# Optimization experiments

Hardware: AMD Instinct MI355X
Metric: run time of the kernel (lower is better)

## Reference

```python
import jax, jax.numpy as jnp
import numpy as np

B, T, C, DK = 4096, 33, 512, 64  # batch, seq (== encoder_block_size), n_embd, d_k


def setup_inputs() -> dict:
    key = jax.random.key(0)
    k1, k2, k3, k4 = jax.random.split(key, 4)
    w_scale = 1.0 / np.sqrt(C).astype(np.float32)
    x = jax.random.normal(k1, (B, T, C), dtype=jnp.float32)
    Wq = jax.random.normal(k2, (DK, C), dtype=jnp.float32) * w_scale
    Wk = jax.random.normal(k3, (DK, C), dtype=jnp.float32) * w_scale
    Wv = jax.random.normal(k4, (DK, C), dtype=jnp.float32) * w_scale
    return {"x": x, "Wq": Wq, "Wk": Wk, "Wv": Wv}


def reference(x, Wq, Wk, Wv):
    # nn.Linear(n_embd, d_k, bias=False): y = x @ W.T
    q = jnp.einsum('btc,dc->btd', x, Wq)  # [B,T,DK]
    k = jnp.einsum('btc,dc->btd', x, Wk)
    v = jnp.einsum('btc,dc->btd', x, Wv)
    # NOTE: original scales by C**-0.5 (n_embd), not d_k**-0.5 — keep faithful.
    wei = jnp.einsum('btd,bsd->bts', q, k) * (C ** -0.5)  # [B,T,T]
    tril = jnp.tril(jnp.ones((T, T), dtype=bool))
    wei = jnp.where(tril, wei, -jnp.inf)
    wei = jax.nn.softmax(wei, axis=-1)
    # dropout p=0.0 -> identity
    out = jnp.einsum('bts,bsd->btd', wei, v)  # [B,T,DK]
    return out
```

## Files before the change

### kernel.cpp

```cpp
#include <hip/hip_runtime.h>
#include <hip/hip_bf16.h>


typedef __attribute__((ext_vector_type(8))) short bf16x8;
typedef __attribute__((ext_vector_type(4))) float floatx4;

#define NB 4096
#define TT 33
#define CC 512

#define CHS 136
#define QS  72
#define OFF_C0 0
#define OFF_C1 8976
#define OFF_Q  0
#define OFF_K  4752
#define OFF_VT 9504
#define OFF_P  18720
#define SMEM_BYTES 25632

__device__ __forceinline__ ushort f2b(float f) {
    union { __hip_bfloat16 h; ushort u; } cv;
    cv.h = __float2bfloat16(f);
    return cv.u;
}
__device__ __forceinline__ int imin(int a, int b) { return a < b ? a : b; }

__device__ __forceinline__ bf16x8 load8_b(const ushort* p) { return *(const bf16x8*)p; }
__device__ __forceinline__ bf16x8 load8_f(const float* p) {
    float4 f0 = *(const float4*)p;
    float4 f1 = *(const float4*)(p + 4);
    bf16x8 r;
    r[0] = (short)f2b(f0.x); r[1] = (short)f2b(f0.y);
    r[2] = (short)f2b(f0.z); r[3] = (short)f2b(f0.w);
    r[4] = (short)f2b(f1.x); r[5] = (short)f2b(f1.y);
    r[6] = (short)f2b(f1.z); r[7] = (short)f2b(f1.w);
    return r;
}

__global__ void conv_w_kernel(const float* __restrict__ Wq,
                              const float* __restrict__ Wk,
                              const float* __restrict__ Wv,
                              ushort* __restrict__ wb) {
    const float* src = (blockIdx.y == 0) ? Wq : (blockIdx.y == 1) ? Wk : Wv;
    int i = (blockIdx.x * 256 + threadIdx.x) * 4;
    float4 f = *(const float4*)&src[i];
    ushort4 u;
    u.x = f2b(f.x); u.y = f2b(f.y); u.z = f2b(f.z); u.w = f2b(f.w);
    *(ushort4*)&wb[(size_t)blockIdx.y * 32768 + i] = u;
}

template <bool USE_WS>
__global__ __launch_bounds__(256, 4) void head_kernel(
    const float* __restrict__ x,
    const ushort* __restrict__ wb,
    const float* __restrict__ Wqf,
    const float* __restrict__ Wkf,
    const float* __restrict__ Wvf,
    float* __restrict__ out)
{
    __shared__ __align__(16) char smem[SMEM_BYTES];
    ushort* xc0  = (ushort*)(smem + OFF_C0);
    ushort* xc1  = (ushort*)(smem + OFF_C1);
    ushort* q_s  = (ushort*)(smem + OFF_Q);
    ushort* k_s  = (ushort*)(smem + OFF_K);
    ushort* vT_s = (ushort*)(smem + OFF_VT);

    const int b    = blockIdx.x;
    const int tid  = threadIdx.x;
    const int lane = tid & 63;
    const int wave = tid >> 6;
    const int l15  = lane & 15;
    const int quad = lane >> 4;

    const float* xg = x + (size_t)b * (TT * CC);

    int nidx[3];
    const ushort* wrow_b[3];
    const float*  wrow_f[3];
    #pragma unroll
    for (int nl = 0; nl < 3; nl++) {
        int n = wave * 3 + nl;
        nidx[nl] = n;
        int mat = n >> 2;
        int row = (n & 3) * 16 + l15;
        if (USE_WS) {
            wrow_b[nl] = wb + (size_t)mat * 32768 + (size_t)row * CC;
            wrow_f[nl] = nullptr;
        } else {
            const float* Wf = (mat == 0) ? Wqf : (mat == 1) ? Wkf : Wvf;
            wrow_f[nl] = Wf + (size_t)row * CC;
            wrow_b[nl] = nullptr;
        }
    }

    float4 buf[5];
    auto LOADCHUNK = [&](int c) {
        #pragma unroll
        for (int j = 0; j < 5; j++) {
            int i = tid + j * 256;
            if (i < 1056) {
                int r = i >> 5, c4 = i & 31;
                buf[j] = ((const float4*)xg)[r * 128 + c * 32 + c4];
            }
        }
    };
    auto WRITECHUNK = [&](ushort* dst) {
        #pragma unroll
        for (int j = 0; j < 5; j++) {
            int i = tid + j * 256;
            if (i < 1056) {
                int r = i >> 5, c4 = i & 31;
                ushort4 u;
                u.x = f2b(buf[j].x); u.y = f2b(buf[j].y);
                u.z = f2b(buf[j].z); u.w = f2b(buf[j].w);
                *(ushort4*)&dst[r * CHS + c4 * 4] = u;
            }
        }
    };

    LOADCHUNK(0);
    WRITECHUNK(xc0);
    __syncthreads();

    floatx4 acc[3][3] = {};
    const int r0 = l15, r1 = 16 + l15, r2 = 32;

    #pragma unroll
    for (int c = 0; c < 4; c++) {
        if (c < 3) LOADCHUNK(c + 1);
        const ushort* xs = (c & 1) ? xc1 : xc0;
        #pragma unroll
        for (int ksl = 0; ksl < 4; ksl++) {
            int col  = ksl * 32 + quad * 8;
            int wcol = c * 128 + col;
            bf16x8 a0 = *(const bf16x8*)&xs[r0 * CHS + col];
            bf16x8 a1 = *(const bf16x8*)&xs[r1 * CHS + col];
            bf16x8 a2 = *(const bf16x8*)&xs[r2 * CHS + col];
            bf16x8 b0 = USE_WS ? load8_b(&wrow_b[0][wcol]) : load8_f(&wrow_f[0][wcol]);
            bf16x8 b1 = USE_WS ? load8_b(&wrow_b[1][wcol]) : load8_f(&wrow_f[1][wcol]);
            bf16x8 b2 = USE_WS ? load8_b(&wrow_b[2][wcol]) : load8_f(&wrow_f[2][wcol]);
            acc[0][0] = __builtin_amdgcn_mfma_f32_16x16x32_bf16(a0, b0, acc[0][0], 0, 0, 0);
            acc[1][0] = __builtin_amdgcn_mfma_f32_16x16x32_bf16(a1, b0, acc[1][0], 0, 0, 0);
            acc[2][0] = __builtin_amdgcn_mfma_f32_16x16x32_bf16(a2, b0, acc[2][0], 0, 0, 0);
            acc[0][1] = __builtin_amdgcn_mfma_f32_16x16x32_bf16(a0, b1, acc[0][1], 0, 0, 0);
            acc[1][1] = __builtin_amdgcn_mfma_f32_16x16x32_bf16(a1, b1, acc[1][1], 0, 0, 0);
            acc[2][1] = __builtin_amdgcn_mfma_f32_16x16x32_bf16(a2, b1, acc[2][1], 0, 0, 0);
            acc[0][2] = __builtin_amdgcn_mfma_f32_16x16x32_bf16(a0, b2, acc[0][2], 0, 0, 0);
            acc[1][2] = __builtin_amdgcn_mfma_f32_16x16x32_bf16(a1, b2, acc[1][2], 0, 0, 0);
            acc[2][2] = __builtin_amdgcn_mfma_f32_16x16x32_bf16(a2, b2, acc[2][2], 0, 0, 0);
        }
        if (c < 3) WRITECHUNK((c & 1) ? xc0 : xc1);
        __syncthreads();
    }

    for (int i = tid; i < 64 * 32; i += 256) {
        int d = i >> 5, t = i & 31;
        if (t) vT_s[d * QS + 32 + t] = 0;
    }
    #pragma unroll
    for (int nl = 0; nl < 3; nl++) {
        int n = nidx[nl];
        int mat = n >> 2;
        int col = (n & 3) * 16 + l15;
        #pragma unroll
        for (int m = 0; m < 3; m++) {
            #pragma unroll
            for (int r = 0; r < 4; r++) {
                int row = m * 16 + quad * 4 + r;
                if (row < TT) {
                    ushort v = f2b(acc[m][nl][r]);
                    if (mat == 0)      q_s[row * QS + col] = v;
                    else if (mat == 1) k_s[row * QS + col] = v;
                    else               vT_s[col * QS + row] = v;
                }
            }
        }
    }
    __syncthreads();

    if (wave >= 3) return;
    const int rowbase = wave * 16;
    ushort* Pw = (ushort*)(smem + OFF_P) + wave * (16 * QS);

    int qr = imin(rowbase + l15, 32);
    bf16x8 aq0 = *(const bf16x8*)&q_s[qr * QS + quad * 8];
    bf16x8 aq1 = *(const bf16x8*)&q_s[qr * QS + 32 + quad * 8];
    floatx4 s[3] = {};
    #pragma unroll
    for (int nt = 0; nt < 3; nt++) {
        int kr = imin(nt * 16 + l15, 32);
        bf16x8 bk0 = *(const bf16x8*)&k_s[kr * QS + quad * 8];
        bf16x8 bk1 = *(const bf16x8*)&k_s[kr * QS + 32 + quad * 8];
        s[nt] = __builtin_amdgcn_mfma_f32_16x16x32_bf16(aq0, bk0, s[nt], 0, 0, 0);
        s[nt] = __builtin_amdgcn_mfma_f32_16x16x32_bf16(aq1, bk1, s[nt], 0, 0, 0);
    }

    const float scale = 0.044194173824159216f;
    #pragma unroll
    for (int nt = 0; nt < 3; nt++)
        #pragma unroll
        for (int r = 0; r < 4; r++) {
            int row = rowbase + quad * 4 + r;
            int col = nt * 16 + l15;
            float v = s[nt][r] * scale;
            s[nt][r] = (col <= row) ? v : -1e30f;
        }
    float inv_s[4];
    #pragma unroll
    for (int r = 0; r < 4; r++) {
        float m = fmaxf(fmaxf(s[0][r], s[1][r]), s[2][r]);
        #pragma unroll
        for (int d = 1; d < 16; d <<= 1) m = fmaxf(m, __shfl_xor(m, d));
        float sum = 0.f;
        #pragma unroll
        for (int nt = 0; nt < 3; nt++) {
            float e = __expf(s[nt][r] - m);
            s[nt][r] = e;
            sum += e;
        }
        #pragma unroll
        for (int d = 1; d < 16; d <<= 1) sum += __shfl_xor(sum, d);
        inv_s[r] = 1.f / sum;
    }

    for (int i = lane; i < 16 * 8; i += 64) {
        int r = i >> 3, c = 48 + ((i & 7) << 1);
        *(uint*)&Pw[r * QS + c] = 0u;
    }
    #pragma unroll
    for (int nt = 0; nt < 3; nt++)
        #pragma unroll
        for (int r = 0; r < 4; r++)
            Pw[(quad * 4 + r) * QS + nt * 16 + l15] = f2b(s[nt][r]);

    bf16x8 ap0 = *(const bf16x8*)&Pw[l15 * QS + quad * 8];
    bf16x8 ap1 = *(const bf16x8*)&Pw[l15 * QS + 32 + quad * 8];
    float* og = out + (size_t)b * (TT * 64);
    #pragma unroll
    for (int nt2 = 0; nt2 < 4; nt2++) {
        int dcol = nt2 * 16 + l15;
        bf16x8 bv0 = *(const bf16x8*)&vT_s[dcol * QS + quad * 8];
        bf16x8 bv1 = *(const bf16x8*)&vT_s[dcol * QS + 32 + quad * 8];
        floatx4 o = {};
        o = __builtin_amdgcn_mfma_f32_16x16x32_bf16(ap0, bv0, o, 0, 0, 0);
        o = __builtin_amdgcn_mfma_f32_16x16x32_bf16(ap1, bv1, o, 0, 0, 0);
        #pragma unroll
        for (int r = 0; r < 4; r++) {
            int row = rowbase + quad * 4 + r;
            if (row < TT) og[row * 64 + dcol] = o[r] * inv_s[r];
        }
    }
}

extern "C" void kernel_launch(void* const* d_in, const int* in_sizes, int n_in,
                              void* d_out, int out_size, void* d_ws, size_t ws_size,
                              hipStream_t stream) {
    const float* x  = (const float*)d_in[0];
    const float* Wq = (const float*)d_in[1];
    const float* Wk = (const float*)d_in[2];
    const float* Wv = (const float*)d_in[3];
    float* out = (float*)d_out;

    if (ws_size >= 3u * 64u * 512u * sizeof(ushort)) {
        ushort* wb = (ushort*)d_ws;
        conv_w_kernel<<<dim3(32, 3), 256, 0, stream>>>(Wq, Wk, Wv, wb);
        head_kernel<true><<<NB, 256, 0, stream>>>(x, wb, nullptr, nullptr, nullptr, out);
    } else {
        head_kernel<false><<<NB, 256, 0, stream>>>(x, nullptr, Wq, Wk, Wv, out);
    }
}
```

Measured before the change: 430.7 us.

## Stream x tile into LDS via async global_load_lds with swizzle and staged waits

Replaces register-staged fp32 load, bf16 convert and LDS write of x chunks with direct global-to-LDS DMA of the full fp32 x tile, XOR-swizzled against bank conflicts, and converts to bf16 when fragments are read for the MFMA. All four chunks are issued up front and consumed in phases gated by vmcnt waits and barriers, overlapping loads with compute. LDS use grows to about 66 KB, so launch bounds drop to 2 blocks per CU, which lowers occupancy and adds conversion work inside the inner loop.

```diff
diff --git a/kernel.cpp b/kernel.cpp
--- a/kernel.cpp
+++ b/kernel.cpp
@@ -9,15 +9,13 @@
 #define TT 33
 #define CC 512
 
-#define CHS 136
-#define QS  72
-#define OFF_C0 0
-#define OFF_C1 8976
-#define OFF_Q  0
-#define OFF_K  4752
-#define OFF_VT 9504
-#define OFF_P  18720
-#define SMEM_BYTES 25632
+#define OFF_Q   0
+#define OFF_K   4752
+#define OFF_VT  9504
+#define OFF_P   18720
+#define X32_OFF 65536
+#define SMEM_BYTES 67584
+#define QS 72
 
 __device__ __forceinline__ ushort f2b(float f) {
     union { __hip_bfloat16 h; ushort u; } cv;
@@ -27,15 +25,22 @@
 __device__ __forceinline__ int imin(int a, int b) { return a < b ? a : b; }
 
 __device__ __forceinline__ bf16x8 load8_b(const ushort* p) { return *(const bf16x8*)p; }
-__device__ __forceinline__ bf16x8 load8_f(const float* p) {
-    float4 f0 = *(const float4*)p;
-    float4 f1 = *(const float4*)(p + 4);
+__device__ __forceinline__ bf16x8 cvt8(float4 f0, float4 f1) {
     bf16x8 r;
     r[0] = (short)f2b(f0.x); r[1] = (short)f2b(f0.y);
     r[2] = (short)f2b(f0.z); r[3] = (short)f2b(f0.w);
     r[4] = (short)f2b(f1.x); r[5] = (short)f2b(f1.y);
     r[6] = (short)f2b(f1.z); r[7] = (short)f2b(f1.w);
     return r;
+}
+__device__ __forceinline__ bf16x8 load8_f(const float* p) {
+    return cvt8(*(const float4*)p, *(const float4*)(p + 4));
+}
+
+__device__ __forceinline__ void dma16(const void* g, void* l) {
+    __builtin_amdgcn_global_load_lds(
+        (const __attribute__((address_space(1))) void*)g,
+        (__attribute__((address_space(3))) void*)l, 16, 0, 0);
 }
 
 __global__ void conv_w_kernel(const float* __restrict__ Wq,
@@ -51,7 +56,7 @@
 }
 
 template <bool USE_WS>
-__global__ __launch_bounds__(256, 4) void head_kernel(
+__global__ __launch_bounds__(256, 2) void head_kernel(
     const float* __restrict__ x,
     const ushort* __restrict__ wb,
     const float* __restrict__ Wqf,
@@ -60,8 +65,6 @@
     float* __restrict__ out)
 {
     __shared__ __align__(16) char smem[SMEM_BYTES];
-    ushort* xc0  = (ushort*)(smem + OFF_C0);
-    ushort* xc1  = (ushort*)(smem + OFF_C1);
     ushort* q_s  = (ushort*)(smem + OFF_Q);
     ushort* k_s  = (ushort*)(smem + OFF_K);
     ushort* vT_s = (ushort*)(smem + OFF_VT);
@@ -73,7 +76,25 @@
     const int l15  = lane & 15;
     const int quad = lane >> 4;
 
-    const float* xg = x + (size_t)b * (TT * CC);
+    const float*  xg  = x + (size_t)b * (TT * CC);
+    const float4* xg4 = (const float4*)xg;
+
+    if (wave < 2) {
+        int cc = 2 * wave + (lane >> 5);
+        dma16(xg4 + 32 * 128 + cc * 32 + (lane & 31),
+              smem + X32_OFF + wave * 1024);
+    }
+    #pragma unroll
+    for (int c = 0; c < 4; c++) {
+        #pragma unroll
+        for (int t = 0; t < 4; t++) {
+            int idx = wave * 256 + t * 64 + lane;
+            int r  = idx >> 5;
+            int lu = (idx & 31) ^ (r & 7);
+            dma16(xg4 + r * 128 + c * 32 + lu,
+                  smem + c * 16384 + wave * 4096 + t * 1024);
+        }
+    }
 
     int nidx[3];
     const ushort* wrow_b[3];
@@ -94,49 +115,26 @@
         }
     }
 
-    float4 buf[5];
-    auto LOADCHUNK = [&](int c) {
-        #pragma unroll
-        for (int j = 0; j < 5; j++) {
-            int i = tid + j * 256;
-            if (i < 1056) {
-                int r = i >> 5, c4 = i & 31;
-                buf[j] = ((const float4*)xg)[r * 128 + c * 32 + c4];
-            }
-        }
-    };
-    auto WRITECHUNK = [&](ushort* dst) {
-        #pragma unroll
-        for (int j = 0; j < 5; j++) {
-            int i = tid + j * 256;
-            if (i < 1056) {
-                int r = i >> 5, c4 = i & 31;
-                ushort4 u;
-                u.x = f2b(buf[j].x); u.y = f2b(buf[j].y);
-                u.z = f2b(buf[j].z); u.w = f2b(buf[j].w);
-                *(ushort4*)&dst[r * CHS + c4 * 4] = u;
-            }
-        }
-    };
-
-    LOADCHUNK(0);
-    WRITECHUNK(xc0);
-    __syncthreads();
-
     floatx4 acc[3][3] = {};
-    const int r0 = l15, r1 = 16 + l15, r2 = 32;
-
-    #pragma unroll
-    for (int c = 0; c < 4; c++) {
-        if (c < 3) LOADCHUNK(c + 1);
-        const ushort* xs = (c & 1) ? xc1 : xc0;
+
+    auto qkv_chunk = [&](int c) {
         #pragma unroll
         for (int ksl = 0; ksl < 4; ksl++) {
-            int col  = ksl * 32 + quad * 8;
-            int wcol = c * 128 + col;
-            bf16x8 a0 = *(const bf16x8*)&xs[r0 * CHS + col];
-            bf16x8 a1 = *(const bf16x8*)&xs[r1 * CHS + col];
-            bf16x8 a2 = *(const bf16x8*)&xs[r2 * CHS + col];
+            int u0 = ksl * 8 + quad * 2;
+            int sw = (u0 ^ (l15 & 7)) << 4;
+            const char* base0 = smem + c * 16384 + l15 * 512;
+            float4 a0lo = *(const float4*)(base0 + sw);
+            float4 a0hi = *(const float4*)(base0 + (sw ^ 16));
+            const char* base1 = base0 + 16 * 512;
+            float4 a1lo = *(const float4*)(base1 + sw);
+            float4 a1hi = *(const float4*)(base1 + (sw ^ 16));
+            const char* base2 = smem + X32_OFF + c * 512 + (u0 << 4);
+            float4 a2lo = *(const float4*)(base2);
+            float4 a2hi = *(const float4*)(base2 + 16);
+            bf16x8 a0 = cvt8(a0lo, a0hi);
+            bf16x8 a1 = cvt8(a1lo, a1hi);
+            bf16x8 a2 = cvt8(a2lo, a2hi);
+            int wcol = c * 128 + ksl * 32 + quad * 8;
             bf16x8 b0 = USE_WS ? load8_b(&wrow_b[0][wcol]) : load8_f(&wrow_f[0][wcol]);
             bf16x8 b1 = USE_WS ? load8_b(&wrow_b[1][wcol]) : load8_f(&wrow_f[1][wcol]);
             bf16x8 b2 = USE_WS ? load8_b(&wrow_b[2][wcol]) : load8_f(&wrow_f[2][wcol]);
@@ -150,9 +148,21 @@
             acc[1][2] = __builtin_amdgcn_mfma_f32_16x16x32_bf16(a1, b2, acc[1][2], 0, 0, 0);
             acc[2][2] = __builtin_amdgcn_mfma_f32_16x16x32_bf16(a2, b2, acc[2][2], 0, 0, 0);
         }
-        if (c < 3) WRITECHUNK((c & 1) ? xc0 : xc1);
-        __syncthreads();
-    }
+    };
+
+#define PHASE(c, VM)                                              \
+    asm volatile("s_waitcnt vmcnt(" #VM ")" ::: "memory");        \
+    __builtin_amdgcn_s_barrier();                                 \
+    asm volatile("" ::: "memory");                                \
+    qkv_chunk(c);
+
+    PHASE(0, 12)
+    PHASE(1, 8)
+    PHASE(2, 4)
+    PHASE(3, 0)
+#undef PHASE
+
+    __syncthreads();
 
     for (int i = tid; i < 64 * 32; i += 256) {
         int d = i >> 5, t = i & 31;
```

Result: slower. 461.8 us (+7.2%).
